# Performance work log

Hardware: AMD Instinct MI355X
Metric: run time of the kernel (lower is better)

Reference implementation:

```python
import jax, jax.numpy as jnp
import numpy as np

B, TE, TD, HE, HD = 8, 256, 256, 512, 512


def setup_inputs() -> dict:
    key = jax.random.key(0)
    k1, k2, k3, k4, k5 = jax.random.split(key, 5)
    return {
        "encoder_out_seq": jax.random.normal(k1, (B, TE, HE), dtype=jnp.float32),
        "decoder_out_seq": jax.random.normal(k2, (B, TD, HD), dtype=jnp.float32),
        "W_a": jax.random.normal(k3, (HE, HE), dtype=jnp.float32) * 0.05,
        "U_a": jax.random.normal(k4, (HD, HE), dtype=jnp.float32) * 0.05,
        "V_a": jax.random.normal(k5, (HE, 1), dtype=jnp.float32) * 0.05,
    }


def reference(encoder_out_seq, decoder_out_seq, W_a, U_a, V_a):
    # Bahdanau additive attention, vectorized over all decoder timesteps.
    # Hoist encoder projection (the K.rnn version recomputed this each step).
    Ws = jnp.einsum('bth,hk->btk', encoder_out_seq, W_a)      # [B, Te, He]
    Uh = jnp.einsum('bdh,hk->bdk', decoder_out_seq, U_a)     # [B, Td, He]
    # tanh(S.Wa + hj.Ua) -> score via V_a, softmax over encoder axis Te
    scores = jnp.einsum('bdtk,k->bdt',
                        jnp.tanh(Ws[:, None, :, :] + Uh[:, :, None, :]),
                        V_a[:, 0])                            # [B, Td, Te]
    e = jax.nn.softmax(scores, axis=-1)                       # energies
    c = jnp.einsum('bdt,bth->bdh', e, encoder_out_seq)        # contexts [B, Td, He]
    return c, e
```

## Files before the change

kernel.cpp:

```cpp
#include <hip/hip_runtime.h>
#include <hip/hip_bf16.h>


#define BB  8
#define TEE 256
#define TDD 256
#define HH  512
#define C2LOG2E 2.8853900817779268f

typedef __attribute__((ext_vector_type(8))) short  short8;
typedef __attribute__((ext_vector_type(4))) float  floatx4;

__device__ __forceinline__ unsigned short f2bf(float f) {
  __hip_bfloat16 h = __float2bfloat16(f);
  return __builtin_bit_cast(unsigned short, h);
}

__global__ __launch_bounds__(256) void prep_proj(
    const float* __restrict__ enc, const float* __restrict__ dec,
    const float* __restrict__ Wa,  const float* __restrict__ Ua,
    float* __restrict__ EW4, float* __restrict__ EU,
    unsigned short* __restrict__ encT)
{
  __shared__ float tile[64][68];
  const int bid = blockIdx.x;
  const int tid = threadIdx.x;

  if (bid < 512) {
    const int side = bid >> 8;
    const int lb = bid & 255;
    const float* X = side ? dec : enc;
    const float* W = side ? Ua  : Wa;
    const int lane = tid & 63, w = tid >> 6;
    const int m0b = (lb >> 3) * 64;
    const int m0 = m0b + w * 16;
    const int n0 = (lb & 7) * 64;
    const int r15 = lane & 15, g = lane >> 4;

    floatx4 acc[4] = {{0.f,0.f,0.f,0.f},{0.f,0.f,0.f,0.f},
                      {0.f,0.f,0.f,0.f},{0.f,0.f,0.f,0.f}};
    const float* ap = X + (size_t)(m0 + r15) * HH + g * 8;

    for (int k0 = 0; k0 < HH; k0 += 32) {
      float4 a0 = *(const float4*)(ap + k0);
      float4 a1 = *(const float4*)(ap + k0 + 4);
      short8 a;
      a[0]=(short)f2bf(a0.x*C2LOG2E); a[1]=(short)f2bf(a0.y*C2LOG2E);
      a[2]=(short)f2bf(a0.z*C2LOG2E); a[3]=(short)f2bf(a0.w*C2LOG2E);
      a[4]=(short)f2bf(a1.x*C2LOG2E); a[5]=(short)f2bf(a1.y*C2LOG2E);
      a[6]=(short)f2bf(a1.z*C2LOG2E); a[7]=(short)f2bf(a1.w*C2LOG2E);
      const float* wrow = W + (size_t)(k0 + g * 8) * HH + n0 + r15;
      #pragma unroll
      for (int nt = 0; nt < 4; ++nt) {
        short8 bv;
        #pragma unroll
        for (int j = 0; j < 8; ++j) bv[j] = (short)f2bf(wrow[(size_t)j * HH + nt * 16]);
        acc[nt] = __builtin_amdgcn_mfma_f32_16x16x32_bf16(a, bv, acc[nt], 0, 0, 0);
      }
    }
    if (side == 1) {
      #pragma unroll
      for (int nt = 0; nt < 4; ++nt) {
        float* yp = EU + (size_t)(m0 + g * 4) * HH + n0 + nt * 16 + r15;
        #pragma unroll
        for (int r = 0; r < 4; ++r) {
          float v = fminf(fmaxf(acc[nt][r], -15.f), 15.f);
          yp[(size_t)r * HH] = __builtin_amdgcn_exp2f(v);
        }
      }
    } else {
      #pragma unroll
      for (int nt = 0; nt < 4; ++nt) {
        #pragma unroll
        for (int r = 0; r < 4; ++r) {
          float v = fminf(fmaxf(acc[nt][r], -15.f), 15.f);
          tile[w * 16 + g * 4 + r][nt * 16 + r15] = __builtin_amdgcn_exp2f(v);
        }
      }
      __syncthreads();
      #pragma unroll
      for (int i = 0; i < 4; ++i) {
        const int cell = i * 256 + tid;
        const int tl  = cell & 63;
        const int k4l = cell >> 6;
        const int m   = m0b + tl;
        const int b   = m >> 8, t = m & 255;
        const int k4  = (n0 >> 2) + k4l;
        float4 val = *(const float4*)&tile[tl][k4l * 4];
        *(float4*)(EW4 + (size_t)b * 131072 + (size_t)k4 * 1024 + t * 4) = val;
      }
    }
  } else {
    const int idx = bid - 512;
    const int b  = idx >> 5;
    const int h0 = ((idx >> 2) & 7) * 64;
    const int t0 = (idx & 3) * 64;
    const int c = tid & 63, r4 = tid >> 6;
    #pragma unroll
    for (int i = 0; i < 16; ++i) {
      int tr = i * 4 + r4;
      tile[tr][c] = enc[((size_t)b * TEE + t0 + tr) * HH + h0 + c];
    }
    __syncthreads();
    #pragma unroll
    for (int i = 0; i < 16; ++i) {
      int hr = i * 4 + r4;
      encT[((size_t)b * HH + h0 + hr) * TEE + t0 + c] = f2bf(tile[c][hr]);
    }
  }
}

__global__ __launch_bounds__(512, 2) void fused(
    const float* __restrict__ EW4, const float* __restrict__ EU,
    const float* __restrict__ Va, const unsigned short* __restrict__ encT,
    float* __restrict__ c_out, float* __restrict__ e_out)
{
  __shared__ float euL[8][512];
  __shared__ float As[8][260];
  __shared__ unsigned short pe[8][264];

  const int bid = blockIdx.x;
  const int b  = bid >> 5;
  const int d0 = (bid & 31) * 8;
  const int tid = threadIdx.x;
  const int t  = tid & 255;
  const int kh = tid >> 8;

  {
    const int dr = tid >> 6, kk = (tid & 63) * 8;
    const float* src = EU + ((size_t)(b * TDD) + d0 + dr) * HH + kk;
    float4 u0 = *(const float4*)(src);
    float4 u1 = *(const float4*)(src + 4);
    *(float4*)&euL[dr][kk]     = u0;
    *(float4*)&euL[dr][kk + 4] = u1;
  }
  __syncthreads();

  float acc[8] = {};
  const float* ewp = EW4 + (size_t)b * 131072 + (size_t)kh * 64 * 1024 + t * 4;
  const float* vap = Va + kh * 256;
  const int kb = kh * 256;

  #pragma unroll 2
  for (int kg = 0; kg < 64; ++kg) {
    float4 ew = *(const float4*)(ewp + (size_t)kg * 1024);
    float4 v  = *(const float4*)(vap + kg * 4);
    #pragma unroll
    for (int d = 0; d < 8; ++d) {
      float4 u = *(const float4*)&euL[d][kb + kg * 4];
      float A1 = fmaf(ew.x, u.x, 1.0f);
      float B1 = fmaf(ew.y, u.y, 1.0f);
      float C1 = fmaf(ew.z, u.z, 1.0f);
      float D1 = fmaf(ew.w, u.w, 1.0f);
      float dab = A1 * B1;
      float nab = fmaf(v.x, B1, v.y * A1);
      float dcd = C1 * D1;
      float ncd = fmaf(v.z, D1, v.w * C1);
      float den = dab * dcd;
      float num = fmaf(nab, dcd, ncd * dab);
      acc[d] = fmaf(num, __builtin_amdgcn_rcpf(den), acc[d]);
    }
  }

  if (kh == 0) {
    #pragma unroll
    for (int d = 0; d < 8; ++d) As[d][t] = acc[d];
  }
  __syncthreads();
  if (kh == 1) {
    #pragma unroll
    for (int d = 0; d < 8; ++d) As[d][t] += acc[d];
  }
  __syncthreads();

  const int w = tid >> 6, lane = tid & 63;
  {
    float4 x = *(const float4*)&As[w][lane * 4];
    float m = fminf(fminf(x.x, x.y), fminf(x.z, x.w));
    #pragma unroll
    for (int off = 32; off; off >>= 1) m = fminf(m, __shfl_xor(m, off));
    float p0 = __builtin_amdgcn_exp2f(C2LOG2E * (m - x.x));
    float p1 = __builtin_amdgcn_exp2f(C2LOG2E * (m - x.y));
    float p2 = __builtin_amdgcn_exp2f(C2LOG2E * (m - x.z));
    float p3 = __builtin_amdgcn_exp2f(C2LOG2E * (m - x.w));
    float s = (p0 + p1) + (p2 + p3);
    #pragma unroll
    for (int off = 32; off; off >>= 1) s += __shfl_xor(s, off);
    float r = __builtin_amdgcn_rcpf(s);
    float4 ev = {p0 * r, p1 * r, p2 * r, p3 * r};
    *(float4*)(e_out + ((size_t)(b * TDD) + d0 + w) * TEE + lane * 4) = ev;
    *(ushort2*)&pe[w][lane * 4]     = make_ushort2(f2bf(ev.x), f2bf(ev.y));
    *(ushort2*)&pe[w][lane * 4 + 2] = make_ushort2(f2bf(ev.z), f2bf(ev.w));
  }
  __syncthreads();

  const int r15 = lane & 15, g = lane >> 4;
  const int hw = w * 64;
  floatx4 ca[4] = {{0.f,0.f,0.f,0.f},{0.f,0.f,0.f,0.f},
                   {0.f,0.f,0.f,0.f},{0.f,0.f,0.f,0.f}};
  const unsigned short* bp0 = encT + ((size_t)b * HH + hw + r15) * TEE + g * 8;

  for (int k0 = 0; k0 < TEE; k0 += 32) {
    short8 a = {0,0,0,0,0,0,0,0};
    if (r15 < 8) a = *(const short8*)&pe[r15][k0 + g * 8];
    #pragma unroll
    for (int nt = 0; nt < 4; ++nt) {
      short8 bv = *(const short8*)(bp0 + (size_t)nt * 16 * TEE + k0);
      ca[nt] = __builtin_amdgcn_mfma_f32_16x16x32_bf16(a, bv, ca[nt], 0, 0, 0);
    }
  }
  if (g < 2) {
    #pragma unroll
    for (int nt = 0; nt < 4; ++nt) {
      float* cp = c_out + ((size_t)(b * TDD) + d0 + g * 4) * HH + hw + nt * 16 + r15;
      #pragma unroll
      for (int r = 0; r < 4; ++r) cp[(size_t)r * HH] = ca[nt][r];
    }
  }
}

extern "C" void kernel_launch(void* const* d_in, const int* in_sizes, int n_in,
                              void* d_out, int out_size, void* d_ws, size_t ws_size,
                              hipStream_t stream) {
  const float* enc = (const float*)d_in[0];
  const float* dec = (const float*)d_in[1];
  const float* Wa  = (const float*)d_in[2];
  const float* Ua  = (const float*)d_in[3];
  const float* Va  = (const float*)d_in[4];

  float* c_out = (float*)d_out;
  float* e_out = c_out + (size_t)BB * TDD * HH;

  float* EW4 = (float*)d_ws;
  float* EU  = EW4 + (size_t)BB * TEE * HH;
  unsigned short* encT = (unsigned short*)(EU + (size_t)BB * TDD * HH);

  prep_proj<<<768, 256, 0, stream>>>(enc, dec, Wa, Ua, EW4, EU, encT);
  fused    <<<256, 512, 0, stream>>>(EW4, EU, Va, encT, c_out, e_out);
}
```

Baseline: 63.92 us.

## Read EU via wave-uniform scalar loads and prefetch EW4 chunks in registers

Removes the shared-memory staging of the decoder projection (euL) and its barrier. Each wave's k-half is now made wave-uniform with readfirstlane, so EU and Va values can be fetched as scalar loads. EW4 is double-buffered in registers four float4 groups at a time, prefetching the next chunk while the current one is computed. The trade-offs are higher register pressure and a dependence on the scalar cache for EU, in exchange for fewer LDS reads and better overlap of the streaming EW4 loads.

```diff
diff --git a/kernel.cpp b/kernel.cpp
--- a/kernel.cpp
+++ b/kernel.cpp
@@ -115,7 +115,6 @@
     const float* __restrict__ Va, const unsigned short* __restrict__ encT,
     float* __restrict__ c_out, float* __restrict__ e_out)
 {
-  __shared__ float euL[8][512];
   __shared__ float As[8][260];
   __shared__ unsigned short pe[8][264];
 
@@ -123,44 +122,55 @@
   const int b  = bid >> 5;
   const int d0 = (bid & 31) * 8;
   const int tid = threadIdx.x;
-  const int t  = tid & 255;
-  const int kh = tid >> 8;
-
-  {
-    const int dr = tid >> 6, kk = (tid & 63) * 8;
-    const float* src = EU + ((size_t)(b * TDD) + d0 + dr) * HH + kk;
-    float4 u0 = *(const float4*)(src);
-    float4 u1 = *(const float4*)(src + 4);
-    *(float4*)&euL[dr][kk]     = u0;
-    *(float4*)&euL[dr][kk + 4] = u1;
-  }
-  __syncthreads();
+  const int lane = tid & 63;
+  const int wu = __builtin_amdgcn_readfirstlane(tid >> 6);
+  const int kh = wu >> 2;
+  const int tq = wu & 3;
+  const int t  = tq * 64 + lane;
 
   float acc[8] = {};
-  const float* ewp = EW4 + (size_t)b * 131072 + (size_t)kh * 64 * 1024 + t * 4;
-  const float* vap = Va + kh * 256;
-  const int kb = kh * 256;
-
-  #pragma unroll 2
-  for (int kg = 0; kg < 64; ++kg) {
-    float4 ew = *(const float4*)(ewp + (size_t)kg * 1024);
-    float4 v  = *(const float4*)(vap + kg * 4);
-    #pragma unroll
+  const float* ewbase = EW4 + (size_t)b * 131072 + (size_t)(kh * 64) * 1024 + t * 4;
+  const float* eub = EU + ((size_t)(b * TDD) + d0) * HH + kh * 256;
+  const float* vab = Va + kh * 256;
+
+#define TREE(EW_, UP_, VP_, AC_) { \
+    float A1 = fmaf(EW_.x, (UP_)[0], 1.0f); \
+    float B1 = fmaf(EW_.y, (UP_)[1], 1.0f); \
+    float C1 = fmaf(EW_.z, (UP_)[2], 1.0f); \
+    float D1 = fmaf(EW_.w, (UP_)[3], 1.0f); \
+    float dab = A1 * B1, dcd = C1 * D1; \
+    float nab = fmaf((VP_)[0], B1, (VP_)[1] * A1); \
+    float ncd = fmaf((VP_)[2], D1, (VP_)[3] * C1); \
+    float den = dab * dcd; \
+    float num = fmaf(nab, dcd, ncd * dab); \
+    AC_ = fmaf(num, __builtin_amdgcn_rcpf(den), AC_); }
+
+  float4 ew0 = *(const float4*)(ewbase);
+  float4 ew1 = *(const float4*)(ewbase + 1024);
+  float4 ew2 = *(const float4*)(ewbase + 2048);
+  float4 ew3 = *(const float4*)(ewbase + 3072);
+
+  for (int c = 0; c < 16; ++c) {
+    float4 n0, n1, n2, n3;
+    if (c + 1 < 16) {
+      const float* p = ewbase + (size_t)(c + 1) * 4096;
+      n0 = *(const float4*)(p);
+      n1 = *(const float4*)(p + 1024);
+      n2 = *(const float4*)(p + 2048);
+      n3 = *(const float4*)(p + 3072);
+    }
+    const float* vp = vab + c * 16;
+    #pragma unroll 2
     for (int d = 0; d < 8; ++d) {
-      float4 u = *(const float4*)&euL[d][kb + kg * 4];
-      float A1 = fmaf(ew.x, u.x, 1.0f);
-      float B1 = fmaf(ew.y, u.y, 1.0f);
-      float C1 = fmaf(ew.z, u.z, 1.0f);
-      float D1 = fmaf(ew.w, u.w, 1.0f);
-      float dab = A1 * B1;
-      float nab = fmaf(v.x, B1, v.y * A1);
-      float dcd = C1 * D1;
-      float ncd = fmaf(v.z, D1, v.w * C1);
-      float den = dab * dcd;
-      float num = fmaf(nab, dcd, ncd * dab);
-      acc[d] = fmaf(num, __builtin_amdgcn_rcpf(den), acc[d]);
-    }
-  }
+      const float* up = eub + (size_t)d * HH + c * 16;
+      TREE(ew0, up,      vp,      acc[d])
+      TREE(ew1, up + 4,  vp + 4,  acc[d])
+      TREE(ew2, up + 8,  vp + 8,  acc[d])
+      TREE(ew3, up + 12, vp + 12, acc[d])
+    }
+    ew0 = n0; ew1 = n1; ew2 = n2; ew3 = n3;
+  }
+#undef TREE
 
   if (kh == 0) {
     #pragma unroll
@@ -173,9 +183,8 @@
   }
   __syncthreads();
 
-  const int w = tid >> 6, lane = tid & 63;
   {
-    float4 x = *(const float4*)&As[w][lane * 4];
+    float4 x = *(const float4*)&As[wu][lane * 4];
     float m = fminf(fminf(x.x, x.y), fminf(x.z, x.w));
     #pragma unroll
     for (int off = 32; off; off >>= 1) m = fminf(m, __shfl_xor(m, off));
@@ -188,14 +197,14 @@
     for (int off = 32; off; off >>= 1) s += __shfl_xor(s, off);
     float r = __builtin_amdgcn_rcpf(s);
     float4 ev = {p0 * r, p1 * r, p2 * r, p3 * r};
-    *(float4*)(e_out + ((size_t)(b * TDD) + d0 + w) * TEE + lane * 4) = ev;
-    *(ushort2*)&pe[w][lane * 4]     = make_ushort2(f2bf(ev.x), f2bf(ev.y));
-    *(ushort2*)&pe[w][lane * 4 + 2] = make_ushort2(f2bf(ev.z), f2bf(ev.w));
+    *(float4*)(e_out + ((size_t)(b * TDD) + d0 + wu) * TEE + lane * 4) = ev;
+    *(ushort2*)&pe[wu][lane * 4]     = make_ushort2(f2bf(ev.x), f2bf(ev.y));
+    *(ushort2*)&pe[wu][lane * 4 + 2] = make_ushort2(f2bf(ev.z), f2bf(ev.w));
   }
   __syncthreads();
 
   const int r15 = lane & 15, g = lane >> 4;
-  const int hw = w * 64;
+  const int hw = wu * 64;
   floatx4 ca[4] = {{0.f,0.f,0.f,0.f},{0.f,0.f,0.f,0.f},
                    {0.f,0.f,0.f,0.f},{0.f,0.f,0.f,0.f}};
   const unsigned short* bp0 = encT + ((size_t)b * HH + hw + r15) * TEE + g * 8;
```

After: 103.0 us. +61.2%, slower.

## Split score loop into four K-quarters with two t per thread and prefetch

Applied to the files above, without the earlier changes.

The additive-score loop now splits the hidden dimension into four quarters instead of two. Each thread handles two encoder positions (t and t+128), so every shared-memory load of the decoder projection and V_a vector is reused twice. The next iteration's EW4 values are loaded one step ahead in software, and the partial sums are reduced through a four-slice shared buffer in a single pass, which removes one barrier. In exchange, register pressure rises with 16 accumulators plus the prefetch registers, and shared-memory usage grows, which may limit occupancy under the two-blocks-per-SM launch bound.

```diff
diff --git a/kernel.cpp b/kernel.cpp
--- a/kernel.cpp
+++ b/kernel.cpp
@@ -116,66 +116,76 @@
     float* __restrict__ c_out, float* __restrict__ e_out)
 {
   __shared__ float euL[8][512];
-  __shared__ float As[8][260];
+  __shared__ float As4[4][8][260];
   __shared__ unsigned short pe[8][264];
 
   const int bid = blockIdx.x;
   const int b  = bid >> 5;
   const int d0 = (bid & 31) * 8;
   const int tid = threadIdx.x;
-  const int t  = tid & 255;
-  const int kh = tid >> 8;
+  const int lane = tid & 63;
+  const int kq = tid >> 7;
+  const int tl = tid & 127;
 
   {
-    const int dr = tid >> 6, kk = (tid & 63) * 8;
+    const int dr = tid >> 6, kk = lane * 8;
     const float* src = EU + ((size_t)(b * TDD) + d0 + dr) * HH + kk;
-    float4 u0 = *(const float4*)(src);
-    float4 u1 = *(const float4*)(src + 4);
-    *(float4*)&euL[dr][kk]     = u0;
-    *(float4*)&euL[dr][kk + 4] = u1;
+    *(float4*)&euL[dr][kk]     = *(const float4*)(src);
+    *(float4*)&euL[dr][kk + 4] = *(const float4*)(src + 4);
   }
   __syncthreads();
 
-  float acc[8] = {};
-  const float* ewp = EW4 + (size_t)b * 131072 + (size_t)kh * 64 * 1024 + t * 4;
-  const float* vap = Va + kh * 256;
-  const int kb = kh * 256;
-
-  #pragma unroll 2
-  for (int kg = 0; kg < 64; ++kg) {
-    float4 ew = *(const float4*)(ewp + (size_t)kg * 1024);
-    float4 v  = *(const float4*)(vap + kg * 4);
+#define TREE(EW_, U_, V_, AC_) { \
+    float A1 = fmaf(EW_.x, U_.x, 1.0f); \
+    float B1 = fmaf(EW_.y, U_.y, 1.0f); \
+    float C1 = fmaf(EW_.z, U_.z, 1.0f); \
+    float D1 = fmaf(EW_.w, U_.w, 1.0f); \
+    float dab = A1 * B1, dcd = C1 * D1; \
+    float nab = fmaf(V_.x, B1, V_.y * A1); \
+    float ncd = fmaf(V_.z, D1, V_.w * C1); \
+    AC_ = fmaf(fmaf(nab, dcd, ncd * dab), \
+               __builtin_amdgcn_rcpf(dab * dcd), AC_); }
+
+  float acc[8][2] = {};
+  const float* ewp = EW4 + (size_t)b * 131072 + (size_t)(kq * 32) * 1024 + tl * 4;
+  const float* vap = Va + kq * 128;
+  const int kb = kq * 128;
+
+  float4 ew0 = *(const float4*)(ewp);
+  float4 ew1 = *(const float4*)(ewp + 512);
+
+  for (int kg = 0; kg < 32; ++kg) {
+    float4 n0, n1;
+    if (kg + 1 < 32) {
+      n0 = *(const float4*)(ewp + (size_t)(kg + 1) * 1024);
+      n1 = *(const float4*)(ewp + (size_t)(kg + 1) * 1024 + 512);
+    }
+    float4 v = *(const float4*)(vap + kg * 4);
     #pragma unroll
     for (int d = 0; d < 8; ++d) {
       float4 u = *(const float4*)&euL[d][kb + kg * 4];
-      float A1 = fmaf(ew.x, u.x, 1.0f);
-      float B1 = fmaf(ew.y, u.y, 1.0f);
-      float C1 = fmaf(ew.z, u.z, 1.0f);
-      float D1 = fmaf(ew.w, u.w, 1.0f);
-      float dab = A1 * B1;
-      float nab = fmaf(v.x, B1, v.y * A1);
-      float dcd = C1 * D1;
-      float ncd = fmaf(v.z, D1, v.w * C1);
-      float den = dab * dcd;
-      float num = fmaf(nab, dcd, ncd * dab);
-      acc[d] = fmaf(num, __builtin_amdgcn_rcpf(den), acc[d]);
-    }
-  }
-
-  if (kh == 0) {
-    #pragma unroll
-    for (int d = 0; d < 8; ++d) As[d][t] = acc[d];
+      TREE(ew0, u, v, acc[d][0])
+      TREE(ew1, u, v, acc[d][1])
+    }
+    ew0 = n0; ew1 = n1;
+  }
+#undef TREE
+
+  #pragma unroll
+  for (int d = 0; d < 8; ++d) {
+    As4[kq][d][tl]       = acc[d][0];
+    As4[kq][d][tl + 128] = acc[d][1];
   }
   __syncthreads();
-  if (kh == 1) {
-    #pragma unroll
-    for (int d = 0; d < 8; ++d) As[d][t] += acc[d];
-  }
-  __syncthreads();
-
-  const int w = tid >> 6, lane = tid & 63;
+
+  const int wu = tid >> 6;
   {
-    float4 x = *(const float4*)&As[w][lane * 4];
+    float4 x = {0.f, 0.f, 0.f, 0.f};
+    #pragma unroll
+    for (int s2 = 0; s2 < 4; ++s2) {
+      float4 xs = *(const float4*)&As4[s2][wu][lane * 4];
+      x.x += xs.x; x.y += xs.y; x.z += xs.z; x.w += xs.w;
+    }
     float m = fminf(fminf(x.x, x.y), fminf(x.z, x.w));
     #pragma unroll
     for (int off = 32; off; off >>= 1) m = fminf(m, __shfl_xor(m, off));
@@ -188,14 +198,14 @@
     for (int off = 32; off; off >>= 1) s += __shfl_xor(s, off);
     float r = __builtin_amdgcn_rcpf(s);
     float4 ev = {p0 * r, p1 * r, p2 * r, p3 * r};
-    *(float4*)(e_out + ((size_t)(b * TDD) + d0 + w) * TEE + lane * 4) = ev;
-    *(ushort2*)&pe[w][lane * 4]     = make_ushort2(f2bf(ev.x), f2bf(ev.y));
-    *(ushort2*)&pe[w][lane * 4 + 2] = make_ushort2(f2bf(ev.z), f2bf(ev.w));
+    *(float4*)(e_out + ((size_t)(b * TDD) + d0 + wu) * TEE + lane * 4) = ev;
+    *(ushort2*)&pe[wu][lane * 4]     = make_ushort2(f2bf(ev.x), f2bf(ev.y));
+    *(ushort2*)&pe[wu][lane * 4 + 2] = make_ushort2(f2bf(ev.z), f2bf(ev.w));
   }
   __syncthreads();
 
   const int r15 = lane & 15, g = lane >> 4;
-  const int hw = w * 64;
+  const int hw = wu * 64;
   floatx4 ca[4] = {{0.f,0.f,0.f,0.f},{0.f,0.f,0.f,0.f},
                    {0.f,0.f,0.f,0.f},{0.f,0.f,0.f,0.f}};
   const unsigned short* bp0 = encT + ((size_t)b * HH + hw + r15) * TEE + g * 8;
```

After: 66.54 us. 1.04x slower.
